# Optimization experiments

Hardware: AMD Instinct MI355X
Metric: run time of the kernel (lower is better)

The kernel has to match this reference:

```python
import jax, jax.numpy as jnp
import numpy as np

B, L, QD, H, D = 2, 2048, 1024, 16, 64  # batch, seq, q_dim, heads, head_dim
INNER = H * D


def rms_norm(x, scale):
    # matches torch RMSNorm: mean over last dim in fp32, eps=1e-6, learned scale
    rrms = jax.lax.rsqrt(jnp.mean(x.astype(jnp.float32) ** 2, axis=-1, keepdims=True) + 1e-6)
    return (x * rrms).astype(x.dtype) * scale


def apply_rope(xq, xk, pe):
    # pe: [1,1,L,D//2,2,2] rotation-matrix pairs (FLUX-style)
    def rot(x):
        xs = x.reshape(*x.shape[:-1], D // 2, 1, 2)  # B H L D/2 1 2
        out = pe[..., 0] * xs[..., 0] + pe[..., 1] * xs[..., 1]  # B H L D/2 2
        return out.reshape(x.shape).astype(x.dtype)
    return rot(xq), rot(xk)


def setup_inputs() -> dict:
    key = jax.random.key(0)
    ks = jax.random.split(key, 6)
    s = 0.02
    return {
        "x": jax.random.normal(ks[0], (B, L, QD), jnp.float32),
        "pe": jax.random.normal(ks[1], (1, 1, L, D // 2, 2, 2), jnp.float32),
        "Wq": jax.random.normal(ks[2], (INNER, QD), jnp.float32) * s,
        "Wkv": jax.random.normal(ks[3], (2 * INNER, QD), jnp.float32) * s,
        "Wproj": jax.random.normal(ks[4], (QD, INNER), jnp.float32) * s,
        "bproj": jnp.zeros((QD,), jnp.float32),
        "q_scale": jnp.ones((D,), jnp.float32),
        "k_scale": jnp.ones((D,), jnp.float32),
    }


def reference(x, pe, Wq, Wkv, Wproj, bproj, q_scale, k_scale):
    # q/kv projections (self-attention: context = x)
    q = jnp.einsum('blc,ec->ble', x, Wq).reshape(B, L, H, D).transpose(0, 2, 1, 3)  # B H L D
    kv = jnp.einsum('blc,ec->ble', x, Wkv).reshape(B, L, 2, H, D)  # layout (K H D)
    k = kv[:, :, 0].transpose(0, 2, 1, 3)  # B H L D
    v = kv[:, :, 1].transpose(0, 2, 1, 3)  # B H L D
    # per-head QK RMSNorm
    q = rms_norm(q, q_scale)
    k = rms_norm(k, k_scale)
    # RoPE then scaled dot-product attention
    q, k = apply_rope(q, k, pe)
    scores = jnp.einsum('bhqd,bhkd->bhqk', q, k) / np.float32(np.sqrt(D))
    attn = jax.nn.softmax(scores, axis=-1)
    o = jnp.einsum('bhqk,bhkd->bhqd', attn, v)
    o = o.transpose(0, 2, 1, 3).reshape(B, L, INNER)  # B L (H D)
    return o @ Wproj.T + bproj
```

## Files before the change

kernel.cpp:

```cpp
#include <hip/hip_runtime.h>
#include <hip/hip_bf16.h>
#include <stdint.h>

#define BB 2
#define LL 2048
#define QDIM 1024
#define NH 16
#define HD 64

using bf16x8 = __attribute__((ext_vector_type(8))) __bf16;
using bf16x2 = __attribute__((ext_vector_type(2))) __bf16;
using f32x4  = __attribute__((ext_vector_type(4))) float;
using u16x8  = __attribute__((ext_vector_type(8))) unsigned short;
using u32x2  = __attribute__((ext_vector_type(2))) uint32_t;

__device__ __forceinline__ unsigned short f2bf(float f) {
  return __builtin_bit_cast(unsigned short, (__bf16)f);
}
__device__ __forceinline__ float bf2f(unsigned short h) {
  uint32_t u = ((uint32_t)h) << 16;
  return __builtin_bit_cast(float, u);
}
__device__ __forceinline__ uint32_t pkbf2(float a, float b) {
  bf16x2 v = { (__bf16)a, (__bf16)b };
  return __builtin_bit_cast(uint32_t, v);
}

__device__ __forceinline__ void gload_lds16(const void* g, void* l) {
  __builtin_amdgcn_global_load_lds((__attribute__((address_space(1))) void*)g,
                                   (__attribute__((address_space(3))) void*)l,
                                   16, 0, 0);
}

__global__ __launch_bounds__(256) void k_cast_all(const float* __restrict__ x,
                                                  const float* __restrict__ wq,
                                                  const float* __restrict__ wkv,
                                                  const float* __restrict__ wp,
                                                  unsigned short* __restrict__ xb,
                                                  unsigned short* __restrict__ wall,
                                                  unsigned short* __restrict__ wpb) {
  const int blk = blockIdx.x;
  const float* src; unsigned short* dst; int base;
  if (blk < 2048)      { src = x;   dst = xb;             base = blk; }
  else if (blk < 2560) { src = wq;  dst = wall;           base = blk - 2048; }
  else if (blk < 3584) { src = wkv; dst = wall + 1048576; base = blk - 2560; }
  else                 { src = wp;  dst = wpb;            base = blk - 3584; }
  const int i = base * 2048 + threadIdx.x * 8;
  float4 a = *reinterpret_cast<const float4*>(src + i);
  float4 b = *reinterpret_cast<const float4*>(src + i + 4);
  u16x8 o;
  o[0] = f2bf(a.x); o[1] = f2bf(a.y); o[2] = f2bf(a.z); o[3] = f2bf(a.w);
  o[4] = f2bf(b.x); o[5] = f2bf(b.y); o[6] = f2bf(b.z); o[7] = f2bf(b.w);
  *reinterpret_cast<u16x8*>(dst + i) = o;
}

__global__ __launch_bounds__(256) void k_gemm_qkv(const unsigned short* __restrict__ A,
                                                  const unsigned short* __restrict__ Bw,
                                                  unsigned short* __restrict__ qk,
                                                  unsigned short* __restrict__ vT,
                                                  const float* __restrict__ pe,
                                                  const float* __restrict__ qs,
                                                  const float* __restrict__ ks) {
  __shared__ char smem[32768];
  const int t = threadIdx.x;
  const int lane = t & 63, w = t >> 6;
  const int wm = w >> 1, wn = w & 1;
  const int g = lane >> 4, r16 = lane & 15;
  const size_t am0 = (size_t)blockIdx.x * 128;
  const int bn0 = blockIdx.y * 128;
  const int K = 1024;
  const float S2 = 0.125f * 1.44269504f;

  f32x4 acc[4][4] = {};

  const int o0 = t * 16, row0 = o0 >> 6, cb0 = o0 & 63;
  const int o1 = 4096 + t * 16, row1 = o1 >> 6, cb1 = o1 & 63;

  char* As0 = smem;
  char* Bs0 = smem + 16384;

  gload_lds16(A  + (am0 + row0) * K + (cb0 >> 1), As0 + o0);
  gload_lds16(A  + (am0 + row1) * K + (cb1 >> 1), As0 + o1);
  gload_lds16(Bw + ((size_t)bn0 + row0) * K + (cb0 >> 1), Bs0 + o0);
  gload_lds16(Bw + ((size_t)bn0 + row1) * K + (cb1 >> 1), Bs0 + o1);
  __syncthreads();

  for (int kb = 0; kb < K; kb += 32) {
    const int cur = (kb >> 5) & 1;
    if (kb + 32 < K) {
      const int nxt = cur ^ 1;
      gload_lds16(A  + (am0 + row0) * K + kb + 32 + (cb0 >> 1), As0 + nxt * 8192 + o0);
      gload_lds16(A  + (am0 + row1) * K + kb + 32 + (cb1 >> 1), As0 + nxt * 8192 + o1);
      gload_lds16(Bw + ((size_t)bn0 + row0) * K + kb + 32 + (cb0 >> 1), Bs0 + nxt * 8192 + o0);
      gload_lds16(Bw + ((size_t)bn0 + row1) * K + kb + 32 + (cb1 >> 1), Bs0 + nxt * 8192 + o1);
    }
    bf16x8 af[4], bfr[4];
#pragma unroll
    for (int i = 0; i < 4; ++i)
      af[i] = *reinterpret_cast<const bf16x8*>(As0 + cur * 8192 + (wm * 64 + i * 16 + r16) * 64 + g * 16);
#pragma unroll
    for (int j = 0; j < 4; ++j)
      bfr[j] = *reinterpret_cast<const bf16x8*>(Bs0 + cur * 8192 + (wn * 64 + j * 16 + r16) * 64 + g * 16);
#pragma unroll
    for (int i = 0; i < 4; ++i)
#pragma unroll
      for (int j = 0; j < 4; ++j)
        acc[i][j] = __builtin_amdgcn_mfma_f32_16x16x32_bf16(af[i], bfr[j], acc[i][j], 0, 0, 0);
    __syncthreads();
  }

  if (bn0 < 2048) {
    const bool isQ = (bn0 < 1024);
    float sc[4];
#pragma unroll
    for (int j = 0; j < 4; ++j) {
      const int d = j * 16 + r16;
      sc[j] = isQ ? qs[d] * S2 : ks[d];
    }
#pragma unroll
    for (int i = 0; i < 4; ++i) {
      const size_t rowb = am0 + wm * 64 + i * 16 + g * 4;
      float rr[4];
#pragma unroll
      for (int r = 0; r < 4; ++r) {
        float s = 0.f;
#pragma unroll
        for (int j = 0; j < 4; ++j) s += acc[i][j][r] * acc[i][j][r];
        s += __shfl_xor(s, 1); s += __shfl_xor(s, 2);
        s += __shfl_xor(s, 4); s += __shfl_xor(s, 8);
        rr[r] = rsqrtf(s * (1.0f / 64.0f) + 1e-6f);
      }
#pragma unroll
      for (int j = 0; j < 4; ++j) {
        const int d = j * 16 + r16;
        const int dp = d >> 1, odd = d & 1;
        const int col = bn0 + wn * 64 + d;
#pragma unroll
        for (int r = 0; r < 4; ++r) {
          const int l = (int)((rowb + r) & (LL - 1));
          float v = acc[i][j][r] * rr[r] * sc[j];
          float pr = __shfl_xor(v, 1);
          float xe = odd ? pr : v, xo = odd ? v : pr;
          const float2 pe2 = *reinterpret_cast<const float2*>(pe + ((size_t)l * 32 + dp) * 4 + odd * 2);
          qk[(rowb + r) * 2048 + col] = f2bf(pe2.x * xe + pe2.y * xo);
        }
      }
    }
  } else {
    unsigned short* Tr = (unsigned short*)smem;
#pragma unroll
    for (int i = 0; i < 4; ++i)
#pragma unroll
      for (int j = 0; j < 4; ++j) {
        const int c = wn * 64 + j * 16 + r16;
        const int rw = wm * 64 + i * 16 + g * 4;
        const int byte = c * 256 + ((rw * 2) ^ ((c & 7) << 4));
        u32x2 pk;
        pk[0] = pkbf2(acc[i][j][0], acc[i][j][1]);
        pk[1] = pkbf2(acc[i][j][2], acc[i][j][3]);
        *reinterpret_cast<u32x2*>((char*)Tr + byte) = pk;
      }
    __syncthreads();
    const int b = (int)(am0 >> 11);
    const int lbase = (int)(am0 & (LL - 1));
#pragma unroll
    for (int p = 0; p < 8; ++p) {
      const int c = p * 16 + (t >> 4);
      const int ch = t & 15;
      const int byte = c * 256 + ((ch * 16) ^ ((c & 7) << 4));
      u16x8 val = *reinterpret_cast<const u16x8*>((char*)Tr + byte);
      const int e = bn0 + c - 2048, h = e >> 6, d = e & 63;
      *reinterpret_cast<u16x8*>(vT + ((size_t)(b * 16 + h) * 64 + d) * 2048 + lbase + ch * 8) = val;
    }
  }
}

__global__ __launch_bounds__(256) void k_gemm_proj(const unsigned short* __restrict__ A,
                                                   const unsigned short* __restrict__ Bw,
                                                   float* __restrict__ Cf,
                                                   const float* __restrict__ bias) {
  __shared__ unsigned short As[2][64 * 32];
  __shared__ unsigned short Bs[2][128 * 32];
  const int t = threadIdx.x;
  const int lane = t & 63, w = t >> 6;
  const int wm = w >> 1, wn = w & 1;
  const int g = lane >> 4, r16 = lane & 15;
  const size_t am0 = (size_t)blockIdx.x * 64;
  const size_t bn0 = (size_t)blockIdx.y * 128;
  const int K = 1024;

  f32x4 acc[2][4] = {};

  const int oa = t * 16, rowa = oa >> 6, cba = oa & 63;
  const int ob0 = t * 16, rowb0 = ob0 >> 6, cbb0 = ob0 & 63;
  const int ob1 = 4096 + t * 16, rowb1 = ob1 >> 6, cbb1 = ob1 & 63;

  gload_lds16(A  + (am0 + rowa)  * K + (cba  >> 1), (char*)&As[0][0] + oa);
  gload_lds16(Bw + (bn0 + rowb0) * K + (cbb0 >> 1), (char*)&Bs[0][0] + ob0);
  gload_lds16(Bw + (bn0 + rowb1) * K + (cbb1 >> 1), (char*)&Bs[0][0] + ob1);
  __syncthreads();

  for (int kb = 0; kb < K; kb += 32) {
    const int cur = (kb >> 5) & 1;
    if (kb + 32 < K) {
      const int nxt = cur ^ 1;
      gload_lds16(A  + (am0 + rowa)  * K + kb + 32 + (cba  >> 1), (char*)&As[nxt][0] + oa);
      gload_lds16(Bw + (bn0 + rowb0) * K + kb + 32 + (cbb0 >> 1), (char*)&Bs[nxt][0] + ob0);
      gload_lds16(Bw + (bn0 + rowb1) * K + kb + 32 + (cbb1 >> 1), (char*)&Bs[nxt][0] + ob1);
    }
    bf16x8 af[2], bfr[4];
#pragma unroll
    for (int i = 0; i < 2; ++i)
      af[i] = *reinterpret_cast<const bf16x8*>((const char*)&As[cur][0] + (wm * 32 + i * 16 + r16) * 64 + g * 16);
#pragma unroll
    for (int j = 0; j < 4; ++j)
      bfr[j] = *reinterpret_cast<const bf16x8*>((const char*)&Bs[cur][0] + (wn * 64 + j * 16 + r16) * 64 + g * 16);
#pragma unroll
    for (int i = 0; i < 2; ++i)
#pragma unroll
      for (int j = 0; j < 4; ++j)
        acc[i][j] = __builtin_amdgcn_mfma_f32_16x16x32_bf16(af[i], bfr[j], acc[i][j], 0, 0, 0);
    __syncthreads();
  }

#pragma unroll
  for (int i = 0; i < 2; ++i)
#pragma unroll
    for (int j = 0; j < 4; ++j) {
      size_t row = am0 + wm * 32 + i * 16 + g * 4;
      int col = (int)bn0 + wn * 64 + j * 16 + r16;
#pragma unroll
      for (int r = 0; r < 4; ++r) Cf[(row + r) * 1024 + col] = acc[i][j][r] + bias[col];
    }
}

__global__ __launch_bounds__(256, 2) void k_flash(const unsigned short* __restrict__ qkbuf,
                                                  const unsigned short* __restrict__ vT,
                                                  unsigned short* __restrict__ ob) {
  __shared__ unsigned short Ktile[2][64 * 64];
  __shared__ unsigned short Vtile[2][64 * 64];
  __shared__ unsigned short Plds[4][2][16 * 64];
  const int t = threadIdx.x, w = t >> 6, lane = t & 63;
  const int g = lane >> 4, r16 = lane & 15;
  const int id = blockIdx.x;
  const int bh = (id & 7) + (((id >> 3) & 3) << 3);
  const int lt = id >> 5;
  const int b = bh >> 4, h = bh & 15;
  const int l0 = lt * 128 + w * 16;
  const size_t qkb = (size_t)b * LL * 2048;
  const unsigned short* Qp = qkbuf + qkb + (size_t)(l0 + r16) * 2048 + h * 64;
  const unsigned short* Kbase = qkbuf + qkb + 1024 + h * 64;
  const unsigned short* Vbase = vT + (size_t)bh * 64 * 2048;

  bf16x8 qf[2][2];
  qf[0][0] = *reinterpret_cast<const bf16x8*>(Qp + g * 8);
  qf[0][1] = *reinterpret_cast<const bf16x8*>(Qp + 32 + g * 8);
  qf[1][0] = *reinterpret_cast<const bf16x8*>(Qp + (size_t)64 * 2048 + g * 8);
  qf[1][1] = *reinterpret_cast<const bf16x8*>(Qp + (size_t)64 * 2048 + 32 + g * 8);

  f32x4 oacc[2][4] = {};
  float m[2] = {-1e30f, -1e30f}, lsum[2] = {0.f, 0.f};

  char* Pw0 = (char*)&Plds[w][0][0];
  char* Pw1 = (char*)&Plds[w][1][0];
  const int pswz = (r16 & 7) << 4;
  const int prow = r16 * 128;
  const int wr0 = prow + ((0 * 32 + g * 8) ^ pswz);
  const int wr1 = prow + ((1 * 32 + g * 8) ^ pswz);
  const int wr2 = prow + ((2 * 32 + g * 8) ^ pswz);
  const int wr3 = prow + ((3 * 32 + g * 8) ^ pswz);
  const int rd0 = prow + ((g * 16) ^ pswz);
  const int rd1 = prow + ((64 + g * 16) ^ pswz);

  const int so0 = t * 16, sr0 = so0 >> 7, sl0 = (so0 & 127) ^ ((sr0 & 7) << 4);
  const int so1 = 4096 + t * 16, sr1 = so1 >> 7, sl1 = (so1 & 127) ^ ((sr1 & 7) << 4);

  gload_lds16(Kbase + (size_t)sr0 * 2048 + (sl0 >> 1), (char*)&Ktile[0][0] + so0);
  gload_lds16(Kbase + (size_t)sr1 * 2048 + (sl1 >> 1), (char*)&Ktile[0][0] + so1);
  gload_lds16(Vbase + (size_t)sr0 * 2048 + (sl0 >> 1), (char*)&Vtile[0][0] + so0);
  gload_lds16(Vbase + (size_t)sr1 * 2048 + (sl1 >> 1), (char*)&Vtile[0][0] + so1);
  __syncthreads();

  const int kswz = (r16 & 7) << 4;

  for (int kt = 0; kt < LL; kt += 64) {
    const int cur = (kt >> 6) & 1;
    if (kt + 64 < LL) {
      const int nxt = cur ^ 1;
      gload_lds16(Kbase + (size_t)(kt + 64 + sr0) * 2048 + (sl0 >> 1), (char*)&Ktile[nxt][0] + so0);
      gload_lds16(Kbase + (size_t)(kt + 64 + sr1) * 2048 + (sl1 >> 1), (char*)&Ktile[nxt][0] + so1);
      gload_lds16(Vbase + (size_t)sr0 * 2048 + kt + 64 + (sl0 >> 1), (char*)&Vtile[nxt][0] + so0);
      gload_lds16(Vbase + (size_t)sr1 * 2048 + kt + 64 + (sl1 >> 1), (char*)&Vtile[nxt][0] + so1);
    }
    const char* Kt = (const char*)&Ktile[cur][0];
    const char* Vt = (const char*)&Vtile[cur][0];

    f32x4 s[2][4];
#pragma unroll
    for (int kb = 0; kb < 4; ++kb) {
      const char* kp = Kt + (kb * 16 + r16) * 128;
      bf16x8 ka0 = *reinterpret_cast<const bf16x8*>(kp + ((g * 16) ^ kswz));
      bf16x8 ka1 = *reinterpret_cast<const bf16x8*>(kp + ((64 + g * 16) ^ kswz));
#pragma unroll
      for (int j = 0; j < 2; ++j) {
        f32x4 z = {};
        z = __builtin_amdgcn_mfma_f32_16x16x32_bf16(ka0, qf[j][0], z, 0, 0, 0);
        z = __builtin_amdgcn_mfma_f32_16x16x32_bf16(ka1, qf[j][1], z, 0, 0, 0);
        s[j][kb] = z;
      }
    }
#pragma unroll
    for (int j = 0; j < 2; ++j) {
      float p[16];
#pragma unroll
      for (int kb = 0; kb < 4; ++kb)
#pragma unroll
        for (int r = 0; r < 4; ++r) p[kb * 4 + r] = s[j][kb][r];
      float t0 = fmaxf(fmaxf(p[0], p[1]), p[2]);
      float t1 = fmaxf(fmaxf(p[3], p[4]), p[5]);
      float t2 = fmaxf(fmaxf(p[6], p[7]), p[8]);
      float t3 = fmaxf(fmaxf(p[9], p[10]), p[11]);
      float t4 = fmaxf(fmaxf(p[12], p[13]), p[14]);
      float tm = fmaxf(fmaxf(fmaxf(t0, t1), t2), fmaxf(fmaxf(t3, t4), p[15]));
      tm = fmaxf(tm, __shfl_xor(tm, 16));
      tm = fmaxf(tm, __shfl_xor(tm, 32));
      if (!__all(tm <= m[j] + 11.0f)) {
        float nm = fmaxf(m[j], tm);
        float alpha = __builtin_exp2f(m[j] - nm);
        lsum[j] *= alpha;
#pragma unroll
        for (int dt = 0; dt < 4; ++dt) oacc[j][dt] *= alpha;
        m[j] = nm;
      }
#pragma unroll
      for (int i = 0; i < 16; ++i) p[i] = __builtin_exp2f(p[i] - m[j]);
      float a0 = (p[0] + p[1]) + (p[2] + p[3]);
      float a1 = (p[4] + p[5]) + (p[6] + p[7]);
      float a2 = (p[8] + p[9]) + (p[10] + p[11]);
      float a3 = (p[12] + p[13]) + (p[14] + p[15]);
      float ts = (a0 + a1) + (a2 + a3);
      ts += __shfl_xor(ts, 16);
      ts += __shfl_xor(ts, 32);
      lsum[j] += ts;
      char* Pw = j ? Pw1 : Pw0;
      u32x2 wv;
      wv[0] = pkbf2(p[0],  p[1]);  wv[1] = pkbf2(p[2],  p[3]);
      *reinterpret_cast<u32x2*>(Pw + wr0) = wv;
      wv[0] = pkbf2(p[4],  p[5]);  wv[1] = pkbf2(p[6],  p[7]);
      *reinterpret_cast<u32x2*>(Pw + wr1) = wv;
      wv[0] = pkbf2(p[8],  p[9]);  wv[1] = pkbf2(p[10], p[11]);
      *reinterpret_cast<u32x2*>(Pw + wr2) = wv;
      wv[0] = pkbf2(p[12], p[13]); wv[1] = pkbf2(p[14], p[15]);
      *reinterpret_cast<u32x2*>(Pw + wr3) = wv;
    }
    __asm__ __volatile__("s_waitcnt lgkmcnt(0)" ::: "memory");
    bf16x8 pb[2][2];
    pb[0][0] = *reinterpret_cast<const bf16x8*>(Pw0 + rd0);
    pb[0][1] = *reinterpret_cast<const bf16x8*>(Pw0 + rd1);
    pb[1][0] = *reinterpret_cast<const bf16x8*>(Pw1 + rd0);
    pb[1][1] = *reinterpret_cast<const bf16x8*>(Pw1 + rd1);
#pragma unroll
    for (int dt = 0; dt < 4; ++dt) {
      const char* vp = Vt + (dt * 16 + r16) * 128;
      bf16x8 va0 = *reinterpret_cast<const bf16x8*>(vp + ((g * 16) ^ kswz));
      bf16x8 va1 = *reinterpret_cast<const bf16x8*>(vp + ((64 + g * 16) ^ kswz));
#pragma unroll
      for (int j = 0; j < 2; ++j) {
        oacc[j][dt] = __builtin_amdgcn_mfma_f32_16x16x32_bf16(va0, pb[j][0], oacc[j][dt], 0, 0, 0);
        oacc[j][dt] = __builtin_amdgcn_mfma_f32_16x16x32_bf16(va1, pb[j][1], oacc[j][dt], 0, 0, 0);
      }
    }
    __syncthreads();
  }

#pragma unroll
  for (int j = 0; j < 2; ++j) {
    const float inv = 1.0f / lsum[j];
    const size_t orow = (size_t)(b * LL + l0 + j * 64 + r16) * 1024 + h * 64;
#pragma unroll
    for (int dt = 0; dt < 4; ++dt) {
      ushort4 pk;
      pk.x = f2bf(oacc[j][dt][0] * inv); pk.y = f2bf(oacc[j][dt][1] * inv);
      pk.z = f2bf(oacc[j][dt][2] * inv); pk.w = f2bf(oacc[j][dt][3] * inv);
      *reinterpret_cast<ushort4*>(ob + orow + dt * 16 + g * 4) = pk;
    }
  }
}

extern "C" void kernel_launch(void* const* d_in, const int* in_sizes, int n_in,
                              void* d_out, int out_size, void* d_ws, size_t ws_size,
                              hipStream_t stream) {
  const float* x     = (const float*)d_in[0];
  const float* pe    = (const float*)d_in[1];
  const float* Wq    = (const float*)d_in[2];
  const float* Wkv   = (const float*)d_in[3];
  const float* Wproj = (const float*)d_in[4];
  const float* bproj = (const float*)d_in[5];
  const float* qs    = (const float*)d_in[6];
  const float* ks    = (const float*)d_in[7];
  float* out = (float*)d_out;

  char* ws = (char*)d_ws;
  unsigned short* xb     = (unsigned short*)(ws);
  unsigned short* Wall   = (unsigned short*)(ws + 8u  * 1024 * 1024);
  unsigned short* Wprojb = (unsigned short*)(ws + 14u * 1024 * 1024);
  unsigned short* qk     = (unsigned short*)(ws + 16u * 1024 * 1024);
  unsigned short* vT     = (unsigned short*)(ws + 32u * 1024 * 1024);
  unsigned short* ob     = (unsigned short*)(ws + 40u * 1024 * 1024);

  k_cast_all<<<4096, 256, 0, stream>>>(x, Wq, Wkv, Wproj, xb, Wall, Wprojb);
  k_gemm_qkv<<<dim3(32, 24), 256, 0, stream>>>(xb, Wall, qk, vT, pe, qs, ks);
  k_flash<<<512, 256, 0, stream>>>(qk, vT, ob);
  k_gemm_proj<<<dim3(64, 8), 256, 0, stream>>>(ob, Wprojb, out, bproj);
}
```

Before: 223.6 us.

## Feed softmax probabilities to PV MFMA directly from registers, bypassing LDS

Removes the per-wave LDS staging buffer for the probability tile. The S accumulator layout is packed straight into bf16 operands for 16x16x16 MFMAs, so P no longer goes through an LDS write, waitcnt and read before the PV product. V is read from LDS as 8-byte fragments instead of 16-byte ones. s_setprio is raised around both MFMA phases to favour matrix issue. The trade is twice as many MFMA instructions (K=16 instead of K=32) and narrower V loads, in exchange for less LDS traffic, a shorter dependency chain and lower LDS use.

```diff
diff --git a/kernel.cpp b/kernel.cpp
--- a/kernel.cpp
+++ b/kernel.cpp
@@ -9,10 +9,12 @@
 #define HD 64
 
 using bf16x8 = __attribute__((ext_vector_type(8))) __bf16;
+using bf16x4 = __attribute__((ext_vector_type(4))) __bf16;
 using bf16x2 = __attribute__((ext_vector_type(2))) __bf16;
 using f32x4  = __attribute__((ext_vector_type(4))) float;
 using u16x8  = __attribute__((ext_vector_type(8))) unsigned short;
 using u32x2  = __attribute__((ext_vector_type(2))) uint32_t;
+using s16x4  = __attribute__((ext_vector_type(4))) short;
 
 __device__ __forceinline__ unsigned short f2bf(float f) {
   return __builtin_bit_cast(unsigned short, (__bf16)f);
@@ -24,6 +26,19 @@
 __device__ __forceinline__ uint32_t pkbf2(float a, float b) {
   bf16x2 v = { (__bf16)a, (__bf16)b };
   return __builtin_bit_cast(uint32_t, v);
+}
+
+__device__ __forceinline__ f32x4 mfma16(u32x2 a, u32x2 b, f32x4 c) {
+#if __has_builtin(__builtin_amdgcn_mfma_f32_16x16x16_bf16)
+  return __builtin_amdgcn_mfma_f32_16x16x16_bf16(__builtin_bit_cast(bf16x4, a),
+                                                 __builtin_bit_cast(bf16x4, b), c, 0, 0, 0);
+#elif __has_builtin(__builtin_amdgcn_mfma_f32_16x16x16bf16_1k)
+  return __builtin_amdgcn_mfma_f32_16x16x16bf16_1k(__builtin_bit_cast(s16x4, a),
+                                                   __builtin_bit_cast(s16x4, b), c, 0, 0, 0);
+#else
+  asm("v_mfma_f32_16x16x16_bf16 %0, %1, %2, %0" : "+v"(c) : "v"(a), "v"(b));
+  return c;
+#endif
 }
 
 __device__ __forceinline__ void gload_lds16(const void* g, void* l) {
@@ -239,7 +254,6 @@
                                                   unsigned short* __restrict__ ob) {
   __shared__ unsigned short Ktile[2][64 * 64];
   __shared__ unsigned short Vtile[2][64 * 64];
-  __shared__ unsigned short Plds[4][2][16 * 64];
   const int t = threadIdx.x, w = t >> 6, lane = t & 63;
   const int g = lane >> 4, r16 = lane & 15;
   const int id = blockIdx.x;
@@ -261,17 +275,6 @@
   f32x4 oacc[2][4] = {};
   float m[2] = {-1e30f, -1e30f}, lsum[2] = {0.f, 0.f};
 
-  char* Pw0 = (char*)&Plds[w][0][0];
-  char* Pw1 = (char*)&Plds[w][1][0];
-  const int pswz = (r16 & 7) << 4;
-  const int prow = r16 * 128;
-  const int wr0 = prow + ((0 * 32 + g * 8) ^ pswz);
-  const int wr1 = prow + ((1 * 32 + g * 8) ^ pswz);
-  const int wr2 = prow + ((2 * 32 + g * 8) ^ pswz);
-  const int wr3 = prow + ((3 * 32 + g * 8) ^ pswz);
-  const int rd0 = prow + ((g * 16) ^ pswz);
-  const int rd1 = prow + ((64 + g * 16) ^ pswz);
-
   const int so0 = t * 16, sr0 = so0 >> 7, sl0 = (so0 & 127) ^ ((sr0 & 7) << 4);
   const int so1 = 4096 + t * 16, sr1 = so1 >> 7, sl1 = (so1 & 127) ^ ((sr1 & 7) << 4);
 
@@ -296,6 +299,7 @@
     const char* Vt = (const char*)&Vtile[cur][0];
 
     f32x4 s[2][4];
+    __builtin_amdgcn_s_setprio(1);
 #pragma unroll
     for (int kb = 0; kb < 4; ++kb) {
       const char* kp = Kt + (kb * 16 + r16) * 128;
@@ -309,6 +313,9 @@
         s[j][kb] = z;
       }
     }
+    __builtin_amdgcn_s_setprio(0);
+
+    u32x2 pbv[2][4];
 #pragma unroll
     for (int j = 0; j < 2; ++j) {
       float p[16];
@@ -342,34 +349,24 @@
       ts += __shfl_xor(ts, 16);
       ts += __shfl_xor(ts, 32);
       lsum[j] += ts;
-      char* Pw = j ? Pw1 : Pw0;
-      u32x2 wv;
-      wv[0] = pkbf2(p[0],  p[1]);  wv[1] = pkbf2(p[2],  p[3]);
-      *reinterpret_cast<u32x2*>(Pw + wr0) = wv;
-      wv[0] = pkbf2(p[4],  p[5]);  wv[1] = pkbf2(p[6],  p[7]);
-      *reinterpret_cast<u32x2*>(Pw + wr1) = wv;
-      wv[0] = pkbf2(p[8],  p[9]);  wv[1] = pkbf2(p[10], p[11]);
-      *reinterpret_cast<u32x2*>(Pw + wr2) = wv;
-      wv[0] = pkbf2(p[12], p[13]); wv[1] = pkbf2(p[14], p[15]);
-      *reinterpret_cast<u32x2*>(Pw + wr3) = wv;
-    }
-    __asm__ __volatile__("s_waitcnt lgkmcnt(0)" ::: "memory");
-    bf16x8 pb[2][2];
-    pb[0][0] = *reinterpret_cast<const bf16x8*>(Pw0 + rd0);
-    pb[0][1] = *reinterpret_cast<const bf16x8*>(Pw0 + rd1);
-    pb[1][0] = *reinterpret_cast<const bf16x8*>(Pw1 + rd0);
-    pb[1][1] = *reinterpret_cast<const bf16x8*>(Pw1 + rd1);
-#pragma unroll
-    for (int dt = 0; dt < 4; ++dt) {
-      const char* vp = Vt + (dt * 16 + r16) * 128;
-      bf16x8 va0 = *reinterpret_cast<const bf16x8*>(vp + ((g * 16) ^ kswz));
-      bf16x8 va1 = *reinterpret_cast<const bf16x8*>(vp + ((64 + g * 16) ^ kswz));
-#pragma unroll
-      for (int j = 0; j < 2; ++j) {
-        oacc[j][dt] = __builtin_amdgcn_mfma_f32_16x16x32_bf16(va0, pb[j][0], oacc[j][dt], 0, 0, 0);
-        oacc[j][dt] = __builtin_amdgcn_mfma_f32_16x16x32_bf16(va1, pb[j][1], oacc[j][dt], 0, 0, 0);
-      }
-    }
+#pragma unroll
+      for (int kb = 0; kb < 4; ++kb) {
+        pbv[j][kb][0] = pkbf2(p[kb * 4 + 0], p[kb * 4 + 1]);
+        pbv[j][kb][1] = pkbf2(p[kb * 4 + 2], p[kb * 4 + 3]);
+      }
+    }
+
+    __builtin_amdgcn_s_setprio(1);
+#pragma unroll
+    for (int kb = 0; kb < 4; ++kb) {
+#pragma unroll
+      for (int dt = 0; dt < 4; ++dt) {
+        u32x2 va = *reinterpret_cast<const u32x2*>(Vt + (dt * 16 + r16) * 128 + ((kb * 32 + g * 8) ^ kswz));
+        oacc[0][dt] = mfma16(va, pbv[0][kb], oacc[0][dt]);
+        oacc[1][dt] = mfma16(va, pbv[1][kb], oacc[1][dt]);
+      }
+    }
+    __builtin_amdgcn_s_setprio(0);
     __syncthreads();
   }
 
```

Result: faster. 218.4 us (-2.3%).
